# Performance work log

Measured on AMD Instinct MI355X. Metric: run time of the kernel, lower is better.

Reference implementation:

```python
import jax, jax.numpy as jnp
import numpy as np

N_NODES = 50000
N_EDGES = 1600000
C_IN = 128
C_OUT = 128


def setup_inputs() -> dict:
    key = jax.random.key(0)
    k1, k2, k3 = jax.random.split(key, 3)
    x = jax.random.normal(k1, (N_NODES, C_IN), dtype=jnp.float32)
    edge_index = jax.random.randint(k2, (2, N_EDGES), 0, N_NODES, dtype=jnp.int64)
    # Glorot-style init for the GCN weight, zero bias (PyG defaults)
    scale = jnp.sqrt(6.0 / (C_IN + C_OUT)).astype(jnp.float32)
    W = jax.random.uniform(k3, (C_IN, C_OUT), dtype=jnp.float32, minval=-scale, maxval=scale)
    b = jnp.zeros((C_OUT,), dtype=jnp.float32)
    return {"x": x, "edge_index": edge_index, "W": W, "b": b}


def reference(x, edge_index, W, b):
    N = x.shape[0]
    # Linear transform first (PyG GCNConv applies lin before propagate)
    h = x @ W  # [N, C_OUT]

    # Add self-loops
    loop = jnp.arange(N, dtype=edge_index.dtype)
    row = jnp.concatenate([edge_index[0], loop])  # source nodes
    col = jnp.concatenate([edge_index[1], loop])  # target nodes

    # Symmetric degree normalization: deg computed at target (col)
    ones = jnp.ones(row.shape[0], dtype=h.dtype)
    deg = jax.ops.segment_sum(ones, col, num_segments=N)  # [N]
    deg_inv_sqrt = jnp.where(deg > 0, jax.lax.rsqrt(deg), 0.0)
    norm = deg_inv_sqrt[row] * deg_inv_sqrt[col]  # [E+N]

    # Gather source features, scale, scatter-add to targets
    msg = h[row] * norm[:, None]  # [E+N, C_OUT]
    out = jax.ops.segment_sum(msg, col, num_segments=N)  # [N, C_OUT]
    out = out + b
    return jax.nn.relu(out)
```

## Files before the change

### kernel.cpp

```cpp
#include <hip/hip_runtime.h>
#include <stdint.h>

#define NCH 128
#define BK_SHIFT 7
#define BK_TGTS 128
#define NBUCK_MAX 512
#define BKT_CAP 5120
#define PT_EDGES 4096
#define BS_CAP 5120

typedef short bf16x8 __attribute__((ext_vector_type(8)));
typedef float f32x4 __attribute__((ext_vector_type(4)));

__device__ __forceinline__ unsigned short f2bf(float f) {
    union { float f; uint32_t u; } v; v.f = f;
    uint32_t u = v.u;
    uint32_t r = u + 0x7fffu + ((u >> 16) & 1u);
    return (unsigned short)(r >> 16);
}
__device__ __forceinline__ float bf2f(unsigned short h) {
    return __uint_as_float((uint32_t)h << 16);
}
__device__ __forceinline__ float bflo(uint32_t u) { return __uint_as_float(u << 16); }
__device__ __forceinline__ float bfhi(uint32_t u) { return __uint_as_float(u & 0xffff0000u); }

__global__ __launch_bounds__(256) void prep_w_kernel(const float* __restrict__ W,
                                                     short* __restrict__ whl,
                                                     int* __restrict__ bcur) {
    if (blockIdx.x == 0) {
        for (int i = threadIdx.x; i < NBUCK_MAX; i += 256) bcur[i] = 0;
    }
    const int idx = blockIdx.x * 256 + threadIdx.x;
    if (idx >= 2048) return;
    const int ko = idx >> 7;
    const int n = idx & 127;
    const int kt = ko >> 2, g = ko & 3;
    const int ct = n >> 4, l16 = n & 15;
    const int row = g * 16 + l16;
    bf16x8 vh, vl;
    #pragma unroll
    for (int e = 0; e < 8; ++e) {
        const float w = W[(size_t)(ko * 8 + e) * NCH + n];
        const unsigned short wh = f2bf(w);
        vh[e] = (short)wh;
        vl[e] = (short)f2bf(w - bf2f(wh));
    }
    *reinterpret_cast<bf16x8*>(&whl[(((0 * 4 + kt) * 8 + ct) * 64 + row) * 8]) = vh;
    *reinterpret_cast<bf16x8*>(&whl[(((1 * 4 + kt) * 8 + ct) * 64 + row) * 8]) = vl;
}

__global__ __launch_bounds__(256) void partition_kernel(const int* __restrict__ ei, int E,
                                                        int nbuck,
                                                        int* __restrict__ bcur,
                                                        uint32_t* __restrict__ bkt) {
    __shared__ int hist[NBUCK_MAX];
    __shared__ int cbase[NBUCK_MAX];
    __shared__ uint32_t stage[PT_EDGES];
    __shared__ int s_is64;
    const int t = threadIdx.x;
    const int e0 = blockIdx.x * PT_EDGES;
    const int cnt = min(PT_EDGES, E - e0);

    if (t == 0) s_is64 = 0;
    for (int i = t; i < NBUCK_MAX; i += 256) hist[i] = 0;
    __syncthreads();
    if (t < 128 && ei[2 * t + 1] != 0) s_is64 = 1;
    __syncthreads();
    const bool is64 = (s_is64 == 0);

    int rank[PT_EDGES / 256];
    #pragma unroll
    for (int j = 0; j < PT_EDGES / 256; ++j) {
        const int i = t + j * 256;
        if (i < cnt) {
            int r, c;
            if (is64) {
                r = reinterpret_cast<const int2*>(ei)[(size_t)(e0 + i)].x;
                c = reinterpret_cast<const int2*>(ei)[(size_t)E + e0 + i].x;
            } else {
                r = ei[e0 + i];
                c = ei[(size_t)E + e0 + i];
            }
            stage[i] = ((uint32_t)c << 16) | (uint32_t)r;
            rank[j] = atomicAdd(&hist[c >> BK_SHIFT], 1);
        }
    }
    __syncthreads();
    for (int b = t; b < nbuck; b += 256) {
        cbase[b] = hist[b] ? atomicAdd(&bcur[b], hist[b]) : 0;
    }
    __syncthreads();
    #pragma unroll
    for (int j = 0; j < PT_EDGES / 256; ++j) {
        const int i = t + j * 256;
        if (i < cnt) {
            const uint32_t p = stage[i];
            const int b = (int)(p >> (16 + BK_SHIFT));
            const int pos = cbase[b] + rank[j];
            if (pos < BKT_CAP) bkt[(size_t)b * BKT_CAP + pos] = p;
        }
    }
}

__global__ __launch_bounds__(256) void bucket_sort_kernel(const uint32_t* __restrict__ bkt,
                                                          const int* __restrict__ bcur,
                                                          int N, int nbuck,
                                                          unsigned short* __restrict__ entries,
                                                          int* __restrict__ offsets,
                                                          float* __restrict__ dinv) {
    __shared__ uint32_t se[BS_CAP];
    __shared__ int hist[BK_TGTS];
    __shared__ int lofs[BK_TGTS];
    __shared__ int s_beg;
    const int b = blockIdx.x;
    const int t = threadIdx.x;
    const int c0 = b << BK_SHIFT;
    const int ntgt = min(BK_TGTS, N - c0);

    for (int i = t; i < BK_TGTS; i += 256) hist[i] = 0;
    if (t < 64) {
        int sum = 0;
        for (int i = t; i < b; i += 64) sum += min(bcur[i], BKT_CAP);
        #pragma unroll
        for (int d = 1; d < 64; d <<= 1) sum += __shfl_xor(sum, d);
        if (t == 0) s_beg = sum;
    }
    __syncthreads();
    const int beg = s_beg;
    const int nE = min(bcur[b], BKT_CAP);
    const uint32_t* win = bkt + (size_t)b * BKT_CAP;

    for (int i = t; i < nE; i += 256) {
        const uint32_t p = win[i];
        se[i] = p;
        atomicAdd(&hist[(int)(p >> 16) - c0], 1);
    }
    __syncthreads();

    if (t < 64) {
        const int h0 = hist[2 * t], h1 = hist[2 * t + 1];
        int s = h0 + h1;
        #pragma unroll
        for (int d = 1; d < 64; d <<= 1) {
            const int u = __shfl_up(s, d);
            if (t >= d) s += u;
        }
        const int ex = s - (h0 + h1);
        lofs[2 * t] = ex;
        lofs[2 * t + 1] = ex + h0;
    }
    __syncthreads();

    for (int i = t; i < ntgt; i += 256) {
        offsets[c0 + i] = beg + lofs[i];
        dinv[c0 + i] = rsqrtf((float)(hist[i] + 1));
    }
    if (t == 0 && b == nbuck - 1) offsets[N] = beg + nE;
    __syncthreads();

    for (int i = t; i < BK_TGTS; i += 256) hist[i] = lofs[i];
    __syncthreads();
    for (int i = t; i < nE; i += 256) {
        const uint32_t p = se[i];
        const int tgt = (int)(p >> 16) - c0;
        const int pos = atomicAdd(&hist[tgt], 1);
        entries[beg + pos] = (unsigned short)(p & 0xffffu);
    }
}

__global__ __launch_bounds__(256) void gemm_xw_mfma_kernel(const float* __restrict__ x,
                                                           const short* __restrict__ whl,
                                                           const float* __restrict__ dinv,
                                                           uint32_t* __restrict__ hb, int N) {
    __shared__ short sW[2][4][8][64][8];
    const int t = threadIdx.x;

    {
        short* d = &sW[0][0][0][0][0];
        #pragma unroll
        for (int i = t * 8; i < 2 * 4 * 8 * 64 * 8; i += 256 * 8)
            *reinterpret_cast<bf16x8*>(d + i) = *reinterpret_cast<const bf16x8*>(whl + i);
    }
    __syncthreads();

    const int wave = t >> 6;
    const int lane = t & 63;
    const int g = lane >> 4;
    const int l16 = lane & 15;
    const int row0 = blockIdx.x * 64 + wave * 16;
    if (row0 >= N) return;
    const int arow = min(row0 + l16, N - 1);

    bf16x8 ah[4], al[4];
    const float* xr = x + (size_t)arow * NCH + g * 8;
    #pragma unroll
    for (int kt = 0; kt < 4; ++kt) {
        const float4 v0 = *reinterpret_cast<const float4*>(xr + kt * 32);
        const float4 v1 = *reinterpret_cast<const float4*>(xr + kt * 32 + 4);
        const float vv[8] = {v0.x, v0.y, v0.z, v0.w, v1.x, v1.y, v1.z, v1.w};
        #pragma unroll
        for (int e = 0; e < 8; ++e) {
            const unsigned short h16 = f2bf(vv[e]);
            const float rem = vv[e] - bf2f(h16);
            ah[kt][e] = (short)h16;
            al[kt][e] = (short)f2bf(rem);
        }
    }

    float dn[4];
    #pragma unroll
    for (int r = 0; r < 4; ++r) dn[r] = dinv[min(row0 + g * 4 + r, N - 1)];

    #pragma unroll
    for (int ct = 0; ct < 8; ++ct) {
        f32x4 acc = {0.f, 0.f, 0.f, 0.f};
        #pragma unroll
        for (int kt = 0; kt < 4; ++kt) {
            const bf16x8 bh = *reinterpret_cast<const bf16x8*>(&sW[0][kt][ct][lane][0]);
            const bf16x8 bl = *reinterpret_cast<const bf16x8*>(&sW[1][kt][ct][lane][0]);
            acc = __builtin_amdgcn_mfma_f32_16x16x32_bf16(ah[kt], bh, acc, 0, 0, 0);
            acc = __builtin_amdgcn_mfma_f32_16x16x32_bf16(al[kt], bh, acc, 0, 0, 0);
            acc = __builtin_amdgcn_mfma_f32_16x16x32_bf16(ah[kt], bl, acc, 0, 0, 0);
        }
        #pragma unroll
        for (int r = 0; r < 4; ++r) {
            const float v = acc[r] * dn[r];
            const float o = __shfl_xor(v, 1);
            const int wrow = row0 + g * 4 + r;
            if ((lane & 1) == 0 && wrow < N) {
                const uint32_t p = (uint32_t)f2bf(v) | ((uint32_t)f2bf(o) << 16);
                hb[(size_t)wrow * (NCH / 2) + ct * 8 + (l16 >> 1)] = p;
            }
        }
    }
}

__global__ __launch_bounds__(256) void spmm_csr_kernel(const uint32_t* __restrict__ hb,
                                                       const unsigned short* __restrict__ entries,
                                                       const int* __restrict__ offsets,
                                                       const float* __restrict__ dinv,
                                                       const float* __restrict__ bias,
                                                       float* __restrict__ out, int N) {
    const int lane = threadIdx.x & 63;
    const int n = blockIdx.x * 4 + (threadIdx.x >> 6);
    if (n >= N) return;

    const int half = lane >> 5;
    const int sl = lane & 31;

    const int beg = offsets[n];
    const int end = offsets[n + 1];
    const int len = end - beg;
    const int cnt0 = min(len, 64);

    int pre = 0;
    if (beg + lane < end) pre = (int)__builtin_nontemporal_load(entries + beg + lane);

    const uint32_t* __restrict__ hbs = hb + sl * 2;
    float a0 = 0.f, a1 = 0.f, a2 = 0.f, a3 = 0.f;

    int j = 0;
    for (; 2 * j + 16 <= cnt0; j += 8) {
        const int i0 = 2 * j + half;
        const int s0 = __shfl(pre, i0);
        const int s1 = __shfl(pre, i0 + 2);
        const int s2 = __shfl(pre, i0 + 4);
        const int s3 = __shfl(pre, i0 + 6);
        const int s4 = __shfl(pre, i0 + 8);
        const int s5 = __shfl(pre, i0 + 10);
        const int s6 = __shfl(pre, i0 + 12);
        const int s7 = __shfl(pre, i0 + 14);
        const uint2 u0 = *reinterpret_cast<const uint2*>(hbs + (size_t)s0 * (NCH / 2));
        const uint2 u1 = *reinterpret_cast<const uint2*>(hbs + (size_t)s1 * (NCH / 2));
        const uint2 u2 = *reinterpret_cast<const uint2*>(hbs + (size_t)s2 * (NCH / 2));
        const uint2 u3 = *reinterpret_cast<const uint2*>(hbs + (size_t)s3 * (NCH / 2));
        const uint2 u4 = *reinterpret_cast<const uint2*>(hbs + (size_t)s4 * (NCH / 2));
        const uint2 u5 = *reinterpret_cast<const uint2*>(hbs + (size_t)s5 * (NCH / 2));
        const uint2 u6 = *reinterpret_cast<const uint2*>(hbs + (size_t)s6 * (NCH / 2));
        const uint2 u7 = *reinterpret_cast<const uint2*>(hbs + (size_t)s7 * (NCH / 2));
        a0 += bflo(u0.x); a1 += bfhi(u0.x); a2 += bflo(u0.y); a3 += bfhi(u0.y);
        a0 += bflo(u1.x); a1 += bfhi(u1.x); a2 += bflo(u1.y); a3 += bfhi(u1.y);
        a0 += bflo(u2.x); a1 += bfhi(u2.x); a2 += bflo(u2.y); a3 += bfhi(u2.y);
        a0 += bflo(u3.x); a1 += bfhi(u3.x); a2 += bflo(u3.y); a3 += bfhi(u3.y);
        a0 += bflo(u4.x); a1 += bfhi(u4.x); a2 += bflo(u4.y); a3 += bfhi(u4.y);
        a0 += bflo(u5.x); a1 += bfhi(u5.x); a2 += bflo(u5.y); a3 += bfhi(u5.y);
        a0 += bflo(u6.x); a1 += bfhi(u6.x); a2 += bflo(u6.y); a3 += bfhi(u6.y);
        a0 += bflo(u7.x); a1 += bfhi(u7.x); a2 += bflo(u7.y); a3 += bfhi(u7.y);
    }
    for (; 2 * j + 8 <= cnt0; j += 4) {
        const int i0 = 2 * j + half;
        const int s0 = __shfl(pre, i0);
        const int s1 = __shfl(pre, i0 + 2);
        const int s2 = __shfl(pre, i0 + 4);
        const int s3 = __shfl(pre, i0 + 6);
        const uint2 u0 = *reinterpret_cast<const uint2*>(hbs + (size_t)s0 * (NCH / 2));
        const uint2 u1 = *reinterpret_cast<const uint2*>(hbs + (size_t)s1 * (NCH / 2));
        const uint2 u2 = *reinterpret_cast<const uint2*>(hbs + (size_t)s2 * (NCH / 2));
        const uint2 u3 = *reinterpret_cast<const uint2*>(hbs + (size_t)s3 * (NCH / 2));
        a0 += bflo(u0.x); a1 += bfhi(u0.x); a2 += bflo(u0.y); a3 += bfhi(u0.y);
        a0 += bflo(u1.x); a1 += bfhi(u1.x); a2 += bflo(u1.y); a3 += bfhi(u1.y);
        a0 += bflo(u2.x); a1 += bfhi(u2.x); a2 += bflo(u2.y); a3 += bfhi(u2.y);
        a0 += bflo(u3.x); a1 += bfhi(u3.x); a2 += bflo(u3.y); a3 += bfhi(u3.y);
    }
    for (; 2 * j < cnt0; ++j) {
        const int i0 = 2 * j + half;
        const int s0 = __shfl(pre, min(i0, 63));
        uint2 u0 = *reinterpret_cast<const uint2*>(hbs + (size_t)s0 * (NCH / 2));
        if (i0 >= cnt0) { u0.x = 0u; u0.y = 0u; }
        a0 += bflo(u0.x); a1 += bfhi(u0.x); a2 += bflo(u0.y); a3 += bfhi(u0.y);
    }
    for (int jj = beg + 64 + half; jj < end; jj += 2) {
        const int s0 = __builtin_nontemporal_load(entries + jj);
        const uint2 u0 = *reinterpret_cast<const uint2*>(hbs + (size_t)s0 * (NCH / 2));
        a0 += bflo(u0.x); a1 += bfhi(u0.x); a2 += bflo(u0.y); a3 += bfhi(u0.y);
    }

    a0 += __shfl_xor(a0, 32);
    a1 += __shfl_xor(a1, 32);
    a2 += __shfl_xor(a2, 32);
    a3 += __shfl_xor(a3, 32);

    const uint2 us = *reinterpret_cast<const uint2*>(hbs + (size_t)n * (NCH / 2));
    a0 += bflo(us.x); a1 += bfhi(us.x); a2 += bflo(us.y); a3 += bfhi(us.y);

    const float s = dinv[n];
    if (half == 0) {
        const float4 bb = reinterpret_cast<const float4*>(bias)[sl];
        f32x4 o;
        o.x = fmaxf(a0 * s + bb.x, 0.f);
        o.y = fmaxf(a1 * s + bb.y, 0.f);
        o.z = fmaxf(a2 * s + bb.z, 0.f);
        o.w = fmaxf(a3 * s + bb.w, 0.f);
        __builtin_nontemporal_store(o, reinterpret_cast<f32x4*>(out + (size_t)n * NCH + sl * 4));
    }
}

extern "C" void kernel_launch(void* const* d_in, const int* in_sizes, int n_in,
                              void* d_out, int out_size, void* d_ws, size_t ws_size,
                              hipStream_t stream) {
    const float* x = (const float*)d_in[0];
    const int* ei = (const int*)d_in[1];
    const float* W = (const float*)d_in[2];
    const float* bias = (const float*)d_in[3];
    float* out = (float*)d_out;

    const int N = in_sizes[0] / NCH;
    const int E = in_sizes[1] / 2;
    const int nbuck = (N + BK_TGTS - 1) >> BK_SHIFT;

    char* w = (char*)d_ws;
    const int padN = (N + 127) & ~127;
    const int padN1 = (N + 1 + 127) & ~127;
    int* offsets = (int*)w;                 w += (size_t)padN1 * 4;
    float* dinv = (float*)w;                w += (size_t)padN * 4;
    int* bcur = (int*)w;                    w += NBUCK_MAX * 4;
    short* whl = (short*)w;                 w += 65536;
    uint32_t* bkt = (uint32_t*)w;
    uint32_t* hb = (uint32_t*)w;            w += (size_t)N * (NCH / 2) * 4;
    unsigned short* entries = (unsigned short*)w;  w += (size_t)E * 2;
    (void)ws_size;

    prep_w_kernel<<<8, 256, 0, stream>>>(W, whl, bcur);
    partition_kernel<<<(E + PT_EDGES - 1) / PT_EDGES, 256, 0, stream>>>(ei, E, nbuck, bcur, bkt);
    bucket_sort_kernel<<<nbuck, 256, 0, stream>>>(bkt, bcur, N, nbuck, entries, offsets, dinv);
    gemm_xw_mfma_kernel<<<(N + 63) / 64, 256, 0, stream>>>(x, whl, dinv, hb, N);
    spmm_csr_kernel<<<(N + 3) / 4, 256, 0, stream>>>(hb, entries, offsets, dinv, bias, out, N);
}
```

Baseline: 114.4 us.

## Vectorize bucket sort loads, double GEMM rows per wave, pack SpMM float adds

The bucket sort now reads packed edge entries four at a time with 128-bit loads for both the histogram and scatter passes. The GEMM has each wave compute two 16-row groups, so every LDS load of W feeds twice the MFMA work, and the grid is halved. The SpMM accumulates into float2 vectors so the compiler can emit packed FP32 adds. The trade-offs are higher register pressure in the GEMM and fewer GEMM blocks in flight.

```diff
diff --git a/kernel.cpp b/kernel.cpp
--- a/kernel.cpp
+++ b/kernel.cpp
@@ -11,6 +11,7 @@
 
 typedef short bf16x8 __attribute__((ext_vector_type(8)));
 typedef float f32x4 __attribute__((ext_vector_type(4)));
+typedef float f32x2 __attribute__((ext_vector_type(2)));
 
 __device__ __forceinline__ unsigned short f2bf(float f) {
     union { float f; uint32_t u; } v; v.f = f;
@@ -23,6 +24,12 @@
 }
 __device__ __forceinline__ float bflo(uint32_t u) { return __uint_as_float(u << 16); }
 __device__ __forceinline__ float bfhi(uint32_t u) { return __uint_as_float(u & 0xffff0000u); }
+__device__ __forceinline__ f32x2 bfpair(uint32_t u) {
+    f32x2 r;
+    r.x = __uint_as_float(u << 16);
+    r.y = __uint_as_float(u & 0xffff0000u);
+    return r;
+}
 
 __global__ __launch_bounds__(256) void prep_w_kernel(const float* __restrict__ W,
                                                      short* __restrict__ whl,
@@ -128,9 +135,18 @@
     __syncthreads();
     const int beg = s_beg;
     const int nE = min(bcur[b], BKT_CAP);
+    const int nE4 = nE & ~3;
     const uint32_t* win = bkt + (size_t)b * BKT_CAP;
 
-    for (int i = t; i < nE; i += 256) {
+    for (int i = t * 4; i < nE4; i += 1024) {
+        const uint4 p = *reinterpret_cast<const uint4*>(win + i);
+        *reinterpret_cast<uint4*>(&se[i]) = p;
+        atomicAdd(&hist[(int)(p.x >> 16) - c0], 1);
+        atomicAdd(&hist[(int)(p.y >> 16) - c0], 1);
+        atomicAdd(&hist[(int)(p.z >> 16) - c0], 1);
+        atomicAdd(&hist[(int)(p.w >> 16) - c0], 1);
+    }
+    for (int i = nE4 + t; i < nE; i += 256) {
         const uint32_t p = win[i];
         se[i] = p;
         atomicAdd(&hist[(int)(p >> 16) - c0], 1);
@@ -160,10 +176,17 @@
 
     for (int i = t; i < BK_TGTS; i += 256) hist[i] = lofs[i];
     __syncthreads();
-    for (int i = t; i < nE; i += 256) {
+    for (int i = t * 4; i < nE4; i += 1024) {
+        const uint4 p = *reinterpret_cast<const uint4*>(&se[i]);
+        int pos;
+        pos = atomicAdd(&hist[(int)(p.x >> 16) - c0], 1); entries[beg + pos] = (unsigned short)(p.x & 0xffffu);
+        pos = atomicAdd(&hist[(int)(p.y >> 16) - c0], 1); entries[beg + pos] = (unsigned short)(p.y & 0xffffu);
+        pos = atomicAdd(&hist[(int)(p.z >> 16) - c0], 1); entries[beg + pos] = (unsigned short)(p.z & 0xffffu);
+        pos = atomicAdd(&hist[(int)(p.w >> 16) - c0], 1); entries[beg + pos] = (unsigned short)(p.w & 0xffffu);
+    }
+    for (int i = nE4 + t; i < nE; i += 256) {
         const uint32_t p = se[i];
-        const int tgt = (int)(p >> 16) - c0;
-        const int pos = atomicAdd(&hist[tgt], 1);
+        const int pos = atomicAdd(&hist[(int)(p >> 16) - c0], 1);
         entries[beg + pos] = (unsigned short)(p & 0xffffu);
     }
 }
@@ -187,49 +210,59 @@
     const int lane = t & 63;
     const int g = lane >> 4;
     const int l16 = lane & 15;
-    const int row0 = blockIdx.x * 64 + wave * 16;
+    const int row0 = blockIdx.x * 128 + wave * 16;
     if (row0 >= N) return;
-    const int arow = min(row0 + l16, N - 1);
-
-    bf16x8 ah[4], al[4];
-    const float* xr = x + (size_t)arow * NCH + g * 8;
+
+    bf16x8 ah[2][4], al[2][4];
+    float dn[2][4];
     #pragma unroll
-    for (int kt = 0; kt < 4; ++kt) {
-        const float4 v0 = *reinterpret_cast<const float4*>(xr + kt * 32);
-        const float4 v1 = *reinterpret_cast<const float4*>(xr + kt * 32 + 4);
-        const float vv[8] = {v0.x, v0.y, v0.z, v0.w, v1.x, v1.y, v1.z, v1.w};
-        #pragma unroll
-        for (int e = 0; e < 8; ++e) {
-            const unsigned short h16 = f2bf(vv[e]);
-            const float rem = vv[e] - bf2f(h16);
-            ah[kt][e] = (short)h16;
-            al[kt][e] = (short)f2bf(rem);
-        }
-    }
-
-    float dn[4];
-    #pragma unroll
-    for (int r = 0; r < 4; ++r) dn[r] = dinv[min(row0 + g * 4 + r, N - 1)];
+    for (int grp = 0; grp < 2; ++grp) {
+        const int rbase = row0 + grp * 64;
+        const int arow = min(rbase + l16, N - 1);
+        const float* xr = x + (size_t)arow * NCH + g * 8;
+        #pragma unroll
+        for (int kt = 0; kt < 4; ++kt) {
+            const float4 v0 = *reinterpret_cast<const float4*>(xr + kt * 32);
+            const float4 v1 = *reinterpret_cast<const float4*>(xr + kt * 32 + 4);
+            const float vv[8] = {v0.x, v0.y, v0.z, v0.w, v1.x, v1.y, v1.z, v1.w};
+            #pragma unroll
+            for (int e = 0; e < 8; ++e) {
+                const unsigned short h16 = f2bf(vv[e]);
+                ah[grp][kt][e] = (short)h16;
+                al[grp][kt][e] = (short)f2bf(vv[e] - bf2f(h16));
+            }
+        }
+        #pragma unroll
+        for (int r = 0; r < 4; ++r) dn[grp][r] = dinv[min(rbase + g * 4 + r, N - 1)];
+    }
 
     #pragma unroll
     for (int ct = 0; ct < 8; ++ct) {
-        f32x4 acc = {0.f, 0.f, 0.f, 0.f};
+        f32x4 accA = {0.f, 0.f, 0.f, 0.f};
+        f32x4 accB = {0.f, 0.f, 0.f, 0.f};
         #pragma unroll
         for (int kt = 0; kt < 4; ++kt) {
             const bf16x8 bh = *reinterpret_cast<const bf16x8*>(&sW[0][kt][ct][lane][0]);
             const bf16x8 bl = *reinterpret_cast<const bf16x8*>(&sW[1][kt][ct][lane][0]);
-            acc = __builtin_amdgcn_mfma_f32_16x16x32_bf16(ah[kt], bh, acc, 0, 0, 0);
-            acc = __builtin_amdgcn_mfma_f32_16x16x32_bf16(al[kt], bh, acc, 0, 0, 0);
-            acc = __builtin_amdgcn_mfma_f32_16x16x32_bf16(ah[kt], bl, acc, 0, 0, 0);
-        }
-        #pragma unroll
-        for (int r = 0; r < 4; ++r) {
-            const float v = acc[r] * dn[r];
-            const float o = __shfl_xor(v, 1);
-            const int wrow = row0 + g * 4 + r;
-            if ((lane & 1) == 0 && wrow < N) {
-                const uint32_t p = (uint32_t)f2bf(v) | ((uint32_t)f2bf(o) << 16);
-                hb[(size_t)wrow * (NCH / 2) + ct * 8 + (l16 >> 1)] = p;
+            accA = __builtin_amdgcn_mfma_f32_16x16x32_bf16(ah[0][kt], bh, accA, 0, 0, 0);
+            accA = __builtin_amdgcn_mfma_f32_16x16x32_bf16(al[0][kt], bh, accA, 0, 0, 0);
+            accA = __builtin_amdgcn_mfma_f32_16x16x32_bf16(ah[0][kt], bl, accA, 0, 0, 0);
+            accB = __builtin_amdgcn_mfma_f32_16x16x32_bf16(ah[1][kt], bh, accB, 0, 0, 0);
+            accB = __builtin_amdgcn_mfma_f32_16x16x32_bf16(al[1][kt], bh, accB, 0, 0, 0);
+            accB = __builtin_amdgcn_mfma_f32_16x16x32_bf16(ah[1][kt], bl, accB, 0, 0, 0);
+        }
+        #pragma unroll
+        for (int grp = 0; grp < 2; ++grp) {
+            const f32x4 acc = grp ? accB : accA;
+            #pragma unroll
+            for (int r = 0; r < 4; ++r) {
+                const float v = acc[r] * dn[grp][r];
+                const float o = __shfl_xor(v, 1);
+                const int wrow = row0 + grp * 64 + g * 4 + r;
+                if ((lane & 1) == 0 && wrow < N) {
+                    const uint32_t p = (uint32_t)f2bf(v) | ((uint32_t)f2bf(o) << 16);
+                    hb[(size_t)wrow * (NCH / 2) + ct * 8 + (l16 >> 1)] = p;
+                }
             }
         }
     }
@@ -257,7 +290,8 @@
     if (beg + lane < end) pre = (int)__builtin_nontemporal_load(entries + beg + lane);
 
     const uint32_t* __restrict__ hbs = hb + sl * 2;
-    float a0 = 0.f, a1 = 0.f, a2 = 0.f, a3 = 0.f;
+    f32x2 acc01 = {0.f, 0.f};
+    f32x2 acc23 = {0.f, 0.f};
 
     int j = 0;
     for (; 2 * j + 16 <= cnt0; j += 8) {
@@ -278,14 +312,14 @@
         const uint2 u5 = *reinterpret_cast<const uint2*>(hbs + (size_t)s5 * (NCH / 2));
         const uint2 u6 = *reinterpret_cast<const uint2*>(hbs + (size_t)s6 * (NCH / 2));
         const uint2 u7 = *reinterpret_cast<const uint2*>(hbs + (size_t)s7 * (NCH / 2));
-        a0 += bflo(u0.x); a1 += bfhi(u0.x); a2 += bflo(u0.y); a3 += bfhi(u0.y);
-        a0 += bflo(u1.x); a1 += bfhi(u1.x); a2 += bflo(u1.y); a3 += bfhi(u1.y);
-        a0 += bflo(u2.x); a1 += bfhi(u2.x); a2 += bflo(u2.y); a3 += bfhi(u2.y);
-        a0 += bflo(u3.x); a1 += bfhi(u3.x); a2 += bflo(u3.y); a3 += bfhi(u3.y);
-        a0 += bflo(u4.x); a1 += bfhi(u4.x); a2 += bflo(u4.y); a3 += bfhi(u4.y);
-        a0 += bflo(u5.x); a1 += bfhi(u5.x); a2 += bflo(u5.y); a3 += bfhi(u5.y);
-        a0 += bflo(u6.x); a1 += bfhi(u6.x); a2 += bflo(u6.y); a3 += bfhi(u6.y);
-        a0 += bflo(u7.x); a1 += bfhi(u7.x); a2 += bflo(u7.y); a3 += bfhi(u7.y);
+        acc01 += bfpair(u0.x); acc23 += bfpair(u0.y);
+        acc01 += bfpair(u1.x); acc23 += bfpair(u1.y);
+        acc01 += bfpair(u2.x); acc23 += bfpair(u2.y);
+        acc01 += bfpair(u3.x); acc23 += bfpair(u3.y);
+        acc01 += bfpair(u4.x); acc23 += bfpair(u4.y);
+        acc01 += bfpair(u5.x); acc23 += bfpair(u5.y);
+        acc01 += bfpair(u6.x); acc23 += bfpair(u6.y);
+        acc01 += bfpair(u7.x); acc23 += bfpair(u7.y);
     }
     for (; 2 * j + 8 <= cnt0; j += 4) {
         const int i0 = 2 * j + half;
@@ -297,24 +331,25 @@
         const uint2 u1 = *reinterpret_cast<const uint2*>(hbs + (size_t)s1 * (NCH / 2));
         const uint2 u2 = *reinterpret_cast<const uint2*>(hbs + (size_t)s2 * (NCH / 2));
         const uint2 u3 = *reinterpret_cast<const uint2*>(hbs + (size_t)s3 * (NCH / 2));
-        a0 += bflo(u0.x); a1 += bfhi(u0.x); a2 += bflo(u0.y); a3 += bfhi(u0.y);
-        a0 += bflo(u1.x); a1 += bfhi(u1.x); a2 += bflo(u1.y); a3 += bfhi(u1.y);
-        a0 += bflo(u2.x); a1 += bfhi(u2.x); a2 += bflo(u2.y); a3 += bfhi(u2.y);
-        a0 += bflo(u3.x); a1 += bfhi(u3.x); a2 += bflo(u3.y); a3 += bfhi(u3.y);
+        acc01 += bfpair(u0.x); acc23 += bfpair(u0.y);
+        acc01 += bfpair(u1.x); acc23 += bfpair(u1.y);
+        acc01 += bfpair(u2.x); acc23 += bfpair(u2.y);
+        acc01 += bfpair(u3.x); acc23 += bfpair(u3.y);
     }
     for (; 2 * j < cnt0; ++j) {
         const int i0 = 2 * j + half;
         const int s0 = __shfl(pre, min(i0, 63));
         uint2 u0 = *reinterpret_cast<const uint2*>(hbs + (size_t)s0 * (NCH / 2));
         if (i0 >= cnt0) { u0.x = 0u; u0.y = 0u; }
-        a0 += bflo(u0.x); a1 += bfhi(u0.x); a2 += bflo(u0.y); a3 += bfhi(u0.y);
+        acc01 += bfpair(u0.x); acc23 += bfpair(u0.y);
     }
     for (int jj = beg + 64 + half; jj < end; jj += 2) {
         const int s0 = __builtin_nontemporal_load(entries + jj);
         const uint2 u0 = *reinterpret_cast<const uint2*>(hbs + (size_t)s0 * (NCH / 2));
-        a0 += bflo(u0.x); a1 += bfhi(u0.x); a2 += bflo(u0.y); a3 += bfhi(u0.y);
-    }
-
+        acc01 += bfpair(u0.x); acc23 += bfpair(u0.y);
+    }
+
+    float a0 = acc01.x, a1 = acc01.y, a2 = acc23.x, a3 = acc23.y;
     a0 += __shfl_xor(a0, 32);
     a1 += __shfl_xor(a1, 32);
     a2 += __shfl_xor(a2, 32);
@@ -363,6 +398,6 @@
     prep_w_kernel<<<8, 256, 0, stream>>>(W, whl, bcur);
     partition_kernel<<<(E + PT_EDGES - 1) / PT_EDGES, 256, 0, stream>>>(ei, E, nbuck, bcur, bkt);
     bucket_sort_kernel<<<nbuck, 256, 0, stream>>>(bkt, bcur, N, nbuck, entries, offsets, dinv);
-    gemm_xw_mfma_kernel<<<(N + 63) / 64, 256, 0, stream>>>(x, whl, dinv, hb, N);
+    gemm_xw_mfma_kernel<<<(N + 127) / 128, 256, 0, stream>>>(x, whl, dinv, hb, N);
     spmm_csr_kernel<<<(N + 3) / 4, 256, 0, stream>>>(hb, entries, offsets, dinv, bias, out, N);
 }
```

After: 109.4 us, median of 3. 4.4% less time.
